# Optimization experiments

Measured on AMD Instinct MI355X. Metric: run time of the kernel, lower is better.

## Reference

```python
import jax, jax.numpy as jnp
import numpy as np
from jax import lax

EPS = 1e-5  # flax BatchNorm default epsilon


def _conv(x, w, b, padding='SAME'):
    y = lax.conv_general_dilated(x, w, (1, 1), padding,
                                 dimension_numbers=('NHWC', 'HWIO', 'NHWC'))
    return y + b


def _maxpool(x, window, strides):
    return lax.reduce_window(x, -jnp.inf, lax.max,
                             (1,) + window + (1,), (1,) + strides + (1,), 'SAME')


def _bn_train(x, scale, bias):
    # training-mode BatchNorm: batch statistics over N,H,W
    m = x.mean(axis=(0, 1, 2))
    v = x.var(axis=(0, 1, 2))
    return (x - m) * lax.rsqrt(v + EPS) * scale + bias


def _lstm(x, wx, wh, b, carry, reverse):
    # x: (B, T, D); flax LSTMCell gate order i, f, g, o; bias lives on the
    # hidden dense in flax but is an equivalent single additive term here.
    xs = jnp.swapaxes(x @ wx + b, 0, 1)  # (T, B, 4H), input GEMM hoisted out of scan

    def step(ch, xt):
        c, h = ch
        g = xt + h @ wh
        i, f, gg, o = jnp.split(g, 4, axis=-1)
        c = jax.nn.sigmoid(f) * c + jax.nn.sigmoid(i) * jnp.tanh(gg)
        h = jax.nn.sigmoid(o) * jnp.tanh(c)
        return (c, h), h

    carry, ys = lax.scan(step, carry, xs, reverse=reverse)
    return carry, jnp.swapaxes(ys, 0, 1)  # (B, T, H)


def _forward(x, conv1_w, conv1_b, conv2_w, conv2_b, conv3_w, conv3_b, bn1_s, bn1_b,
             conv4_w, conv4_b, bn2_s, bn2_b, conv5_w, conv5_b, bn3_s, bn3_b,
             conv6_w, conv6_b, bn4_s, bn4_b, conv7_w, conv7_b, bn5_s, bn5_b,
             wq, bq, wk, bk, wv, bv,
             l1f_wx, l1f_wh, l1f_b, l1r_wx, l1r_wh, l1r_b,
             l2f_wx, l2f_wh, l2f_b, l2r_wx, l2r_wh, l2r_b, wo, bo):
    x = jax.nn.relu(_conv(x, conv1_w, conv1_b))
    x = _maxpool(x, (2, 2), (2, 2))
    x = jax.nn.relu(_conv(x, conv2_w, conv2_b))
    x = _maxpool(x, (2, 2), (2, 2))
    x = jax.nn.relu(_bn_train(_conv(x, conv3_w, conv3_b), bn1_s, bn1_b))
    x = jax.nn.relu(_bn_train(_conv(x, conv4_w, conv4_b), bn2_s, bn2_b))
    x = _maxpool(x, (2, 2), (1, 2))
    x = jax.nn.relu(_bn_train(_conv(x, conv5_w, conv5_b), bn3_s, bn3_b))
    x = jax.nn.relu(_bn_train(_conv(x, conv6_w, conv6_b), bn4_s, bn4_b))
    x = _maxpool(x, (2, 2), (1, 2))
    x = jax.nn.relu(_bn_train(_conv(x, conv7_w, conv7_b, padding='VALID'), bn5_s, bn5_b))
    B = x.shape[0]
    x = x.reshape(B, x.shape[1], -1)  # (B, T=H', W'*512); seq axis is height
    q = x @ wq + bq
    k = x @ wk + bk
    v = x @ wv + bv
    qk = jax.nn.softmax(jnp.einsum('btk,bsk->bts', q, k) / 32.0, axis=-1)
    x = jnp.einsum('btk,bts->bsk', v, qk)
    # stack 1: reverse LSTM deliberately starts from forward's FINAL carry (as in source)
    carry = (jnp.zeros((B, 256), x.dtype), jnp.zeros((B, 256), x.dtype))
    carry, y1 = _lstm(x, l1f_wx, l1f_wh, l1f_b, carry, reverse=False)
    carry, y2 = _lstm(x, l1r_wx, l1r_wh, l1r_b, carry, reverse=True)
    x1 = jnp.concatenate([y1, y2], axis=-1)
    # stack 2
    carry = (jnp.zeros((B, 512), x.dtype), jnp.zeros((B, 512), x.dtype))
    carry, y2b = _lstm(x1, l2f_wx, l2f_wh, l2f_b, carry, reverse=False)
    carry, y3 = _lstm(x1, l2r_wx, l2r_wh, l2r_b, carry, reverse=True)
    x = jnp.concatenate([y3, y2b], axis=-1)
    return x @ wo + bo


def setup_inputs() -> dict:
    key = jax.random.key(0)
    ks = iter(jax.random.split(key, 64))

    def cw(kh, kw, ci, co):
        return jax.random.normal(next(ks), (kh, kw, ci, co), jnp.float32) / np.float32(np.sqrt(kh * kw * ci))

    def dw(i, o):
        return jax.random.normal(next(ks), (i, o), jnp.float32) / np.float32(np.sqrt(i))

    z = lambda *s: jnp.zeros(s, jnp.float32)
    ones = lambda *s: jnp.ones(s, jnp.float32)
    class_nums = 1000
    d_in = 15 * 512  # W'=15 after conv stack, 512 channels
    inp = {
        'x': jax.random.normal(next(ks), (32, 64, 256, 3), jnp.float32),
        'conv1_w': cw(3, 3, 3, 64), 'conv1_b': z(64),
        'conv2_w': cw(3, 3, 64, 128), 'conv2_b': z(128),
        'conv3_w': cw(3, 3, 128, 256), 'conv3_b': z(256), 'bn1_s': ones(256), 'bn1_b': z(256),
        'conv4_w': cw(3, 3, 256, 256), 'conv4_b': z(256), 'bn2_s': ones(256), 'bn2_b': z(256),
        'conv5_w': cw(3, 3, 256, 512), 'conv5_b': z(512), 'bn3_s': ones(512), 'bn3_b': z(512),
        'conv6_w': cw(3, 3, 512, 512), 'conv6_b': z(512), 'bn4_s': ones(512), 'bn4_b': z(512),
        'conv7_w': cw(2, 2, 512, 512), 'conv7_b': z(512), 'bn5_s': ones(512), 'bn5_b': z(512),
        'wq': dw(d_in, 512), 'bq': z(512),
        'wk': dw(d_in, 512), 'bk': z(512),
        'wv': dw(d_in, 512), 'bv': z(512),
        'l1f_wx': dw(512, 4 * 256), 'l1f_wh': dw(256, 4 * 256), 'l1f_b': z(4 * 256),
        'l1r_wx': dw(512, 4 * 256), 'l1r_wh': dw(256, 4 * 256), 'l1r_b': z(4 * 256),
        'l2f_wx': dw(512, 4 * 512), 'l2f_wh': dw(512, 4 * 512), 'l2f_b': z(4 * 512),
        'l2r_wx': dw(512, 4 * 512), 'l2r_wh': dw(512, 4 * 512), 'l2r_b': z(4 * 512),
        'wo': dw(1024, class_nums), 'bo': z(class_nums),
    }
    return inp


def reference(x, conv1_w, conv1_b, conv2_w, conv2_b, conv3_w, conv3_b, bn1_s, bn1_b,
              conv4_w, conv4_b, bn2_s, bn2_b, conv5_w, conv5_b, bn3_s, bn3_b,
              conv6_w, conv6_b, bn4_s, bn4_b, conv7_w, conv7_b, bn5_s, bn5_b,
              wq, bq, wk, bk, wv, bv,
              l1f_wx, l1f_wh, l1f_b, l1r_wx, l1r_wh, l1r_b,
              l2f_wx, l2f_wh, l2f_b, l2r_wx, l2r_wh, l2r_b, wo, bo):
    return _forward(x, conv1_w, conv1_b, conv2_w, conv2_b, conv3_w, conv3_b, bn1_s, bn1_b,
                    conv4_w, conv4_b, bn2_s, bn2_b, conv5_w, conv5_b, bn3_s, bn3_b,
                    conv6_w, conv6_b, bn4_s, bn4_b, conv7_w, conv7_b, bn5_s, bn5_b,
                    wq, bq, wk, bk, wv, bv,
                    l1f_wx, l1f_wh, l1f_b, l1r_wx, l1r_wh, l1r_b,
                    l2f_wx, l2f_wh, l2f_b, l2r_wx, l2r_wh, l2r_b, wo, bo)
```

## Files before the change

### kernel.cpp

```cpp
#include <hip/hip_runtime.h>
#include <math.h>

#define DIV_UP(a,b) (((a)+(b)-1)/(b))

typedef _Float16 half_t;
typedef _Float16 half8 __attribute__((ext_vector_type(8)));
typedef float f32x4 __attribute__((ext_vector_type(4)));

#define FLAG_RELU   1
#define FLAG_OUTF32 2
#define FLAG_SPLITK 4
#define FLAG_ATOMIC 8
#define FLAG_BNSUMS 16

#define GLDS16(src, dst) \
  __builtin_amdgcn_global_load_lds((const __attribute__((address_space(1))) void*)(src), \
                                   (__attribute__((address_space(3))) void*)(dst), 16, 0, 0)

__device__ __forceinline__ float fsig_(float x){ return 1.0f/(1.0f+__expf(-x)); }
__device__ __forceinline__ float ftanh_(float x){
  float ax = fabsf(x);
  float e = __expf(-2.0f*ax);
  float t = (1.0f - e)/(1.0f + e);
  return copysignf(t, x);
}

#define NTP 18
struct TpAll {
  const float* src[NTP];
  half_t* dst[NTP];
  int K[NTP];
  int N[NTP];
  int prefix[NTP+1];
};

__global__ __launch_bounds__(256) void transpose_cvt_all_kernel(TpAll a)
{
  __shared__ float tile[32][33];
  int bid = blockIdx.x;
  int z = 0;
  while (bid >= a.prefix[z+1]) ++z;
  int local = bid - a.prefix[z];
  const float* w = a.src[z];
  half_t* wT = a.dst[z];
  int K = a.K[z], N = a.N[z];
  int tilesX = (N + 31) >> 5;
  int nt = (local % tilesX) * 32;
  int kt = (local / tilesX) * 32;
  int tx = threadIdx.x & 31, ty = threadIdx.x >> 5;
  #pragma unroll
  for (int r = 0; r < 4; ++r) {
    int k = kt + ty + r*8, n = nt + tx;
    tile[ty + r*8][tx] = (k < K && n < N) ? w[(long)k*N + n] : 0.f;
  }
  __syncthreads();
  #pragma unroll
  for (int r = 0; r < 4; ++r) {
    int n = nt + ty + r*8, k = kt + tx;
    if (n < N && k < K) wT[(long)n*K + k] = (half_t)tile[tx][ty + r*8];
  }
}

__global__ __launch_bounds__(256) void conv1_kernel(
    const float* __restrict__ x, const float* __restrict__ w,
    const float* __restrict__ bias, half_t* __restrict__ out)
{
  __shared__ float xs[3][258*3];
  int nb = blockIdx.x;
  int n = nb >> 6, ho = nb & 63;
  int tid = threadIdx.x;
  int co = tid & 63;
  float wreg[27];
  #pragma unroll
  for (int k = 0; k < 27; ++k) wreg[k] = w[k*64 + co];
  float bco = bias[co];
  for (int i = tid; i < 3*258*3; i += 256) {
    int row = i / (258*3); int rem = i % (258*3);
    int col = rem / 3;     int ci  = rem % 3;
    int ih = ho - 1 + row; int iw = col - 1;
    float v = 0.f;
    if (ih >= 0 && ih < 64 && iw >= 0 && iw < 256)
      v = x[(((long)n*64 + ih)*256 + iw)*3 + ci];
    xs[row][col*3 + ci] = v;
  }
  __syncthreads();
  int wave = tid >> 6;
  for (int p = 0; p < 64; ++p) {
    int wo = wave*64 + p;
    float acc = bco;
    #pragma unroll
    for (int kh = 0; kh < 3; ++kh)
      #pragma unroll
      for (int kw = 0; kw < 3; ++kw)
        #pragma unroll
        for (int ci = 0; ci < 3; ++ci)
          acc = fmaf(xs[kh][(wo+kw)*3 + ci], wreg[(kh*3+kw)*3 + ci], acc);
    acc = fmaxf(acc, 0.f);
    out[(((long)n*64 + ho)*256 + wo)*64 + co] = (half_t)acc;
  }
}

struct GOut { const half_t* wT; const float* bias; void* out; };

__global__ __launch_bounds__(256) void mfma_conv_kernel(
    const half_t* __restrict__ x, GOut g0, GOut g1, GOut g2,
    const half_t* __restrict__ zbuf, float* __restrict__ bns,
    int N,int H,int W,int Ci,int Ho,int Wo,int Co,
    int KH,int KW,int padH,int padW,
    int M,int K,int flags,int splitS)
{
  GOut g;
  int ciBeg = 0, ciEnd = Ci;
  if (flags & FLAG_SPLITK) {
    g = g0;
    int span = Ci / splitS;
    ciBeg = blockIdx.z * span;
    ciEnd = ciBeg + span;
  } else {
    g = (blockIdx.z == 0) ? g0 : (blockIdx.z == 1 ? g1 : g2);
  }
  const half_t* __restrict__ wT = g.wT;
  __shared__ half_t As[128*64];
  __shared__ half_t Bs[128*64];
  int tid = threadIdx.x;

  int nbx = gridDim.x, nby = gridDim.y;
  int total = nbx * nby;
  int flat = blockIdx.y * nbx + blockIdx.x;
  int q = total >> 3, r = total & 7;
  int xcd = flat & 7;
  int j = flat >> 3;
  int w = xcd * q + (xcd < r ? xcd : r) + j;
  int m0 = (w / nbx) * 128, n0 = (w % nbx) * 128;

  int wave = tid >> 6, lane = tid & 63;
  int l15 = lane & 15, quad = lane >> 4;
  int x7 = lane & 7;
  int wm = (wave & 1) * 64, wn = (wave >> 1) * 64;

  int rSub = tid >> 3;
  int colHalf = (((tid & 7) ^ (rSub & 7))) * 8;

  int ho_[4], wo_[4], ni_[4]; bool av_[4];
  #pragma unroll
  for (int i = 0; i < 4; ++i) {
    int m = m0 + i*32 + rSub;
    av_[i] = m < M;
    int mm = av_[i] ? m : 0;
    wo_[i] = mm % Wo; int t2 = mm / Wo;
    ho_[i] = t2 % Ho; ni_[i] = t2 / Ho;
  }
  const half_t* bBase[4];
  #pragma unroll
  for (int i = 0; i < 4; ++i) {
    int n = n0 + i*32 + rSub;
    bBase[i] = (n < Co) ? (wT + (long)n*K + colHalf) : nullptr;
  }

  int pch0 = ((quad)     ^ x7) * 8;
  int pch1 = ((4 + quad) ^ x7) * 8;

  f32x4 acc[4][4];
  #pragma unroll
  for (int i = 0; i < 4; ++i)
    #pragma unroll
    for (int j2 = 0; j2 < 4; ++j2)
      acc[i][j2] = (f32x4){0.f, 0.f, 0.f, 0.f};

  int kg = ciBeg;
  for (int kh = 0; kh < KH; ++kh) {
    for (int kw = 0; kw < KW; ++kw) {
      long aOff[4]; bool aval[4];
      #pragma unroll
      for (int i = 0; i < 4; ++i) {
        int ih = ho_[i] - padH + kh, iw = wo_[i] - padW + kw;
        bool ok = av_[i] && ih >= 0 && ih < H && iw >= 0 && iw < W;
        aval[i] = ok;
        aOff[i] = ok ? ((((long)ni_[i]*H + ih)*W + iw)*(long)Ci + colHalf) : 0;
      }
      for (int ci = ciBeg; ci < ciEnd; ci += 64, kg += 64) {
        #pragma unroll
        for (int i = 0; i < 4; ++i) {
          const half_t* sa = aval[i] ? (x + aOff[i] + ci) : zbuf;
          GLDS16(sa, As + i*2048 + wave*512);
          const half_t* sb = bBase[i] ? (bBase[i] + kg) : zbuf;
          GLDS16(sb, Bs + i*2048 + wave*512);
        }
        __syncthreads();
        {
          half8 af[4], bf[4];
          #pragma unroll
          for (int i = 0; i < 4; ++i)
            af[i] = *reinterpret_cast<half8*>(&As[(wm + i*16 + l15)*64 + pch0]);
          #pragma unroll
          for (int j2 = 0; j2 < 4; ++j2)
            bf[j2] = *reinterpret_cast<half8*>(&Bs[(wn + j2*16 + l15)*64 + pch0]);
          #pragma unroll
          for (int i = 0; i < 4; ++i)
            #pragma unroll
            for (int j2 = 0; j2 < 4; ++j2)
              acc[i][j2] = __builtin_amdgcn_mfma_f32_16x16x32_f16(af[i], bf[j2], acc[i][j2], 0, 0, 0);
        }
        {
          half8 af[4], bf[4];
          #pragma unroll
          for (int i = 0; i < 4; ++i)
            af[i] = *reinterpret_cast<half8*>(&As[(wm + i*16 + l15)*64 + pch1]);
          #pragma unroll
          for (int j2 = 0; j2 < 4; ++j2)
            bf[j2] = *reinterpret_cast<half8*>(&Bs[(wn + j2*16 + l15)*64 + pch1]);
          #pragma unroll
          for (int i = 0; i < 4; ++i)
            #pragma unroll
            for (int j2 = 0; j2 < 4; ++j2)
              acc[i][j2] = __builtin_amdgcn_mfma_f32_16x16x32_f16(af[i], bf[j2], acc[i][j2], 0, 0, 0);
        }
        __syncthreads();
      }
    }
  }

  if (flags & FLAG_BNSUMS) {
    float* red = (float*)As;
    #pragma unroll
    for (int j2 = 0; j2 < 4; ++j2) {
      int n = n0 + wn + j2*16 + l15;
      float bv = g.bias[n];
      float s = 0.f, qq = 0.f;
      #pragma unroll
      for (int i = 0; i < 4; ++i)
        #pragma unroll
        for (int rr = 0; rr < 4; ++rr) {
          int m = m0 + wm + i*16 + quad*4 + rr;
          if (m < M) { float v = acc[i][j2][rr] + bv; s += v; qq += v*v; }
        }
      int idx = ((((wave*4 + quad)*16 + l15)*4) + j2)*2;
      red[idx] = s; red[idx+1] = qq;
    }
    __syncthreads();
    if (tid < 128) {
      int hi = tid >> 6;
      int jj = (tid >> 4) & 3, ll = tid & 15;
      float s = 0.f, qq = 0.f;
      #pragma unroll
      for (int w2 = 0; w2 < 2; ++w2)
        #pragma unroll
        for (int qd = 0; qd < 4; ++qd) {
          int idx = (((((hi*2 + w2)*4 + qd)*16 + ll)*4) + jj)*2;
          s += red[idx]; qq += red[idx+1];
        }
      int n = n0 + tid;
      atomicAdd(&bns[n], s);
      atomicAdd(&bns[Co + n], qq);
    }
  }

  #pragma unroll
  for (int i = 0; i < 4; ++i) {
    #pragma unroll
    for (int rr = 0; rr < 4; ++rr) {
      int m = m0 + wm + i*16 + quad*4 + rr;
      if (m >= M) continue;
      #pragma unroll
      for (int j2 = 0; j2 < 4; ++j2) {
        int n = n0 + wn + j2*16 + l15;
        if (n >= Co) continue;
        if (flags & FLAG_ATOMIC) {
          atomicAdd(&((float*)g.out)[(long)m*Co + n], acc[i][j2][rr]);
        } else {
          float v = acc[i][j2][rr] + g.bias[n];
          if (flags & FLAG_RELU) v = fmaxf(v, 0.f);
          if (flags & FLAG_OUTF32) ((float*)g.out)[(long)m*Co + n] = v;
          else ((half_t*)g.out)[(long)m*Co + n] = (half_t)v;
        }
      }
    }
  }
}

__global__ __launch_bounds__(256) void maxpool8_kernel(
    const half_t* __restrict__ x, half_t* __restrict__ out,
    int N,int H,int W,int C,int Ho,int Wo,int sH,int sW)
{
  int C8 = C >> 3;
  long idx = (long)blockIdx.x*256 + threadIdx.x;
  long total8 = (long)N*Ho*Wo*C8;
  if (idx >= total8) return;
  int cb = (int)(idx % C8);
  long pix = idx / C8;
  int wo = (int)(pix % Wo); long t2 = pix / Wo;
  int ho = (int)(t2 % Ho); int n = (int)(t2 / Ho);
  int c = cb * 8;
  float m[8];
  #pragma unroll
  for (int e = 0; e < 8; ++e) m[e] = -INFINITY;
  for (int i = 0; i < 2; ++i) {
    int ih = ho*sH + i;
    if (ih >= H) continue;
    for (int j = 0; j < 2; ++j) {
      int iw = wo*sW + j;
      if (iw >= W) continue;
      half8 v = *reinterpret_cast<const half8*>(x + (((long)n*H + ih)*W + iw)*C + c);
      #pragma unroll
      for (int e = 0; e < 8; ++e) m[e] = fmaxf(m[e], (float)v[e]);
    }
  }
  half8 o;
  #pragma unroll
  for (int e = 0; e < 8; ++e) o[e] = (half_t)m[e];
  *reinterpret_cast<half8*>(out + idx*8) = o;
}

__global__ __launch_bounds__(256) void bn_apply_relu8_kernel(
    half_t* __restrict__ x, const float* __restrict__ sums,
    const float* __restrict__ scale, const float* __restrict__ bias,
    long total8, int C, float invN)
{
  long idx = (long)blockIdx.x*256 + threadIdx.x;
  if (idx >= total8) return;
  int c = (int)((idx*8) % C);
  half8 v = *reinterpret_cast<half8*>(x + idx*8);
  half8 o;
  #pragma unroll
  for (int e = 0; e < 8; ++e) {
    float mean = sums[c+e] * invN;
    float var  = sums[C + c+e] * invN - mean*mean;
    float rstd = rsqrtf(var + 1e-5f);
    float y = ((float)v[e] - mean) * rstd * scale[c+e] + bias[c+e];
    o[e] = (half_t)fmaxf(y, 0.0f);
  }
  *reinterpret_cast<half8*>(x + idx*8) = o;
}

__global__ __launch_bounds__(256) void bn_pool8_kernel(
    const half_t* __restrict__ x, half_t* __restrict__ out,
    const float* __restrict__ sums, const float* __restrict__ scale,
    const float* __restrict__ bias,
    int N,int H,int W,int C,int Ho,int Wo,int sH,int sW, float invN)
{
  int C8 = C >> 3;
  long idx = (long)blockIdx.x*256 + threadIdx.x;
  long total8 = (long)N*Ho*Wo*C8;
  if (idx >= total8) return;
  int cb = (int)(idx % C8);
  long pix = idx / C8;
  int wo = (int)(pix % Wo); long t2 = pix / Wo;
  int ho = (int)(t2 % Ho); int n = (int)(t2 / Ho);
  int c = cb * 8;
  float mean[8], rs[8], bb[8];
  #pragma unroll
  for (int e = 0; e < 8; ++e) {
    mean[e] = sums[c+e] * invN;
    float var = sums[C + c+e] * invN - mean[e]*mean[e];
    rs[e] = rsqrtf(var + 1e-5f) * scale[c+e];
    bb[e] = bias[c+e];
  }
  float m[8];
  #pragma unroll
  for (int e = 0; e < 8; ++e) m[e] = -INFINITY;
  for (int i = 0; i < 2; ++i) {
    int ih = ho*sH + i;
    if (ih >= H) continue;
    for (int j = 0; j < 2; ++j) {
      int iw = wo*sW + j;
      if (iw >= W) continue;
      half8 v = *reinterpret_cast<const half8*>(x + (((long)n*H + ih)*W + iw)*C + c);
      #pragma unroll
      for (int e = 0; e < 8; ++e) {
        float y = fmaxf(((float)v[e] - mean[e]) * rs[e] + bb[e], 0.f);
        m[e] = fmaxf(m[e], y);
      }
    }
  }
  half8 o;
  #pragma unroll
  for (int e = 0; e < 8; ++e) o[e] = (half_t)m[e];
  *reinterpret_cast<half8*>(out + idx*8) = o;
}

__global__ __launch_bounds__(256) void bias_fill_kernel(
    float* __restrict__ out, const float* __restrict__ b0,
    const float* __restrict__ b1, const float* __restrict__ b2, int total)
{
  int idx = blockIdx.x*256 + threadIdx.x;
  if (idx >= total) return;
  int n = idx % 1536;
  float v = (n < 512) ? b0[n] : (n < 1024 ? b1[n-512] : b2[n-1024]);
  out[idx] = v;
}

__global__ __launch_bounds__(256) void attention_kernel(
    const float* __restrict__ qkv, half_t* __restrict__ out,
    int T, int D, int ld)
{
  int b = blockIdx.x;
  int tid = threadIdx.x;
  __shared__ float P[15][16];
  if (tid < T*T) {
    int t = tid / T, s = tid % T;
    const float* qp = qkv + ((long)b*T + t)*ld;
    const float* kp = qkv + ((long)b*T + s)*ld + 512;
    float acc = 0.f;
    for (int d = 0; d < D; d += 4) {
      float4 qv = *reinterpret_cast<const float4*>(qp + d);
      float4 kv = *reinterpret_cast<const float4*>(kp + d);
      acc += qv.x*kv.x + qv.y*kv.y + qv.z*kv.z + qv.w*kv.w;
    }
    P[t][s] = acc * (1.0f/32.0f);
  }
  __syncthreads();
  if (tid < T) {
    float mx = -INFINITY;
    for (int s = 0; s < T; ++s) mx = fmaxf(mx, P[tid][s]);
    float sum = 0.f;
    for (int s = 0; s < T; ++s) { float e = expf(P[tid][s] - mx); P[tid][s] = e; sum += e; }
    float inv = 1.0f / sum;
    for (int s = 0; s < T; ++s) P[tid][s] *= inv;
  }
  __syncthreads();
  for (int idx = tid; idx < T*D; idx += 256) {
    int s = idx / D, kk2 = idx % D;
    float acc = 0.f;
    #pragma unroll
    for (int t = 0; t < 15; ++t)
      acc += qkv[((long)b*T + t)*ld + 1024 + kk2] * P[t][s];
    out[((long)b*T + s)*D + kk2] = (half_t)acc;
  }
}

#define MAXK 512
#define HSROW (MAXK + 8)

template<int N64, int HLOG>
__device__ __forceinline__ void stage_h(
    const unsigned long long* __restrict__ src, half_t (*hs)[HSROW], int tid)
{
  unsigned long long tmp[N64];
  #pragma unroll
  for (int u = 0; u < N64; ++u)
    tmp[u] = __hip_atomic_load(src + tid + u*256, __ATOMIC_RELAXED, __HIP_MEMORY_SCOPE_AGENT);
  #pragma unroll
  for (int u = 0; u < N64; ++u) {
    int idx = tid + u*256;
    int row = idx >> (HLOG - 2);
    int col = (idx & ((1 << (HLOG - 2)) - 1)) * 4;
    *reinterpret_cast<unsigned long long*>(&hs[row][col]) = tmp[u];
  }
}

template<int H>
__global__ __launch_bounds__(256, 1) void lstm_persistent_kernel(
    const float* __restrict__ preF, const float* __restrict__ preR,
    const half_t* __restrict__ whTF, const half_t* __restrict__ whTR,
    half_t* __restrict__ hbuf, half_t* __restrict__ y,
    int* __restrict__ flags, int nblk,
    int ystride, int yoffF, int yoffR)
{
  constexpr int KI = H / 32;
  __shared__ half_t hs[32][HSROW];
  __shared__ float gates[32][133];
  int tid = threadIdx.x;
  int jb0 = blockIdx.x * 32;
  int lane = tid & 63, wave = tid >> 6;
  int l15 = lane & 15, quad = lane >> 4;
  int bb = tid >> 3;
  int jj0 = (tid & 7) * 4;
  constexpr int H4 = 4 * H;

  float cst[4] = {0.f, 0.f, 0.f, 0.f};
  half8 wreg[2][KI];

  auto loadw = [&](const half_t* __restrict__ whT) {
    #pragma unroll
    for (int f = 0; f < 2; ++f) {
      const half_t* wp = whT + (long)(wave*H + jb0 + f*16 + l15)*H + quad*8;
      #pragma unroll
      for (int i = 0; i < KI; ++i)
        wreg[f][i] = *reinterpret_cast<const half8*>(wp + i*32);
    }
  };

  auto loadpv = [&](int s, float (&pv)[16]) {
    const float* pr = (s < 15) ? preF : preR;
    int t = (s < 15) ? s : 29 - s;
    const float* pp = pr + (long)(bb*15 + t)*H4 + jb0 + jj0;
    #pragma unroll
    for (int g = 0; g < 4; ++g) {
      f32x4 v = *reinterpret_cast<const f32x4*>(pp + g*H);
      pv[g*4+0] = v[0]; pv[g*4+1] = v[1]; pv[g*4+2] = v[2]; pv[g*4+3] = v[3];
    }
  };

  loadw(whTF);
  float pv[16];
  loadpv(0, pv);

  for (int s = 0; s < 30; ++s) {
    if (s == 15) loadw(whTR);
    int t = (s < 15) ? s : 29 - s;
    int yoff = (s < 15) ? yoffF : yoffR;

    const unsigned long long* hsrc =
        (const unsigned long long*)(hbuf + (long)(s & 1) * 32 * H);
    if constexpr (H == 512) stage_h<16, 9>(hsrc, hs, tid);
    else                    stage_h<8, 8>(hsrc, hs, tid);
    __syncthreads();

    f32x4 acc00 = {0.f,0.f,0.f,0.f}, acc10 = {0.f,0.f,0.f,0.f};
    f32x4 acc01 = {0.f,0.f,0.f,0.f}, acc11 = {0.f,0.f,0.f,0.f};
    #pragma unroll
    for (int i = 0; i < KI; ++i) {
      half8 a0 = *reinterpret_cast<half8*>(&hs[l15][i*32 + quad*8]);
      half8 a1 = *reinterpret_cast<half8*>(&hs[16 + l15][i*32 + quad*8]);
      acc00 = __builtin_amdgcn_mfma_f32_16x16x32_f16(a0, wreg[0][i], acc00, 0, 0, 0);
      acc10 = __builtin_amdgcn_mfma_f32_16x16x32_f16(a1, wreg[0][i], acc10, 0, 0, 0);
      acc01 = __builtin_amdgcn_mfma_f32_16x16x32_f16(a0, wreg[1][i], acc01, 0, 0, 0);
      acc11 = __builtin_amdgcn_mfma_f32_16x16x32_f16(a1, wreg[1][i], acc11, 0, 0, 0);
    }
    #pragma unroll
    for (int r = 0; r < 4; ++r) {
      gates[quad*4 + r][wave*32 + l15]           = acc00[r];
      gates[16 + quad*4 + r][wave*32 + l15]      = acc10[r];
      gates[quad*4 + r][wave*32 + 16 + l15]      = acc01[r];
      gates[16 + quad*4 + r][wave*32 + 16 + l15] = acc11[r];
    }
    __syncthreads();

    unsigned long long hpack;
    {
      half_t hn[4];
      #pragma unroll
      for (int p = 0; p < 4; ++p) {
        int j = jj0 + p;
        float gi = pv[p]      + gates[bb][j];
        float gf = pv[4 + p]  + gates[bb][32 + j];
        float gg = pv[8 + p]  + gates[bb][64 + j];
        float go = pv[12 + p] + gates[bb][96 + j];
        gi = fsig_(gi); gf = fsig_(gf); gg = ftanh_(gg); go = fsig_(go);
        float cn = gf * cst[p] + gi * gg;
        cst[p] = cn;
        hn[p] = (half_t)(go * ftanh_(cn));
      }
      hpack = *reinterpret_cast<unsigned long long*>(hn);
      half_t* hdst = hbuf + (long)((s + 1) & 1) * 32 * H;
      __hip_atomic_store((unsigned long long*)(hdst + (long)bb*H + jb0 + jj0), hpack,
                         __ATOMIC_RELAXED, __HIP_MEMORY_SCOPE_AGENT);
    }

    if (s < 29) {
      __syncthreads();
      if (tid == 0)
        __hip_atomic_store(&flags[blockIdx.x], s + 1,
                           __ATOMIC_RELAXED, __HIP_MEMORY_SCOPE_AGENT);
      *reinterpret_cast<unsigned long long*>(
          &y[(long)(bb*15 + t)*ystride + yoff + jb0 + jj0]) = hpack;
      loadpv(s + 1, pv);
      if (tid < 64) {
        int target = s + 1;
        for (;;) {
          int vv = (tid < nblk)
            ? __hip_atomic_load(&flags[tid], __ATOMIC_RELAXED, __HIP_MEMORY_SCOPE_AGENT)
            : target;
          if (__all(vv >= target)) break;
        }
      }
      __syncthreads();
    } else {
      *reinterpret_cast<unsigned long long*>(
          &y[(long)(bb*15 + t)*ystride + yoff + jb0 + jj0]) = hpack;
    }
  }
}

extern "C" void kernel_launch(void* const* d_in, const int* in_sizes, int n_in,
                              void* d_out, int out_size, void* d_ws, size_t ws_size,
                              hipStream_t stream)
{
  const float* x       = (const float*)d_in[0];
  const float* c1w     = (const float*)d_in[1];  const float* c1b = (const float*)d_in[2];
  const float* c2w     = (const float*)d_in[3];  const float* c2b = (const float*)d_in[4];
  const float* c3w     = (const float*)d_in[5];  const float* c3b = (const float*)d_in[6];
  const float* bn1s    = (const float*)d_in[7];  const float* bn1b = (const float*)d_in[8];
  const float* c4w     = (const float*)d_in[9];  const float* c4b = (const float*)d_in[10];
  const float* bn2s    = (const float*)d_in[11]; const float* bn2b = (const float*)d_in[12];
  const float* c5w     = (const float*)d_in[13]; const float* c5b = (const float*)d_in[14];
  const float* bn3s    = (const float*)d_in[15]; const float* bn3b = (const float*)d_in[16];
  const float* c6w     = (const float*)d_in[17]; const float* c6b = (const float*)d_in[18];
  const float* bn4s    = (const float*)d_in[19]; const float* bn4b = (const float*)d_in[20];
  const float* c7w     = (const float*)d_in[21]; const float* c7b = (const float*)d_in[22];
  const float* bn5s    = (const float*)d_in[23]; const float* bn5b = (const float*)d_in[24];
  const float* wq      = (const float*)d_in[25]; const float* bq = (const float*)d_in[26];
  const float* wk      = (const float*)d_in[27]; const float* bk = (const float*)d_in[28];
  const float* wv      = (const float*)d_in[29]; const float* bv = (const float*)d_in[30];
  const float* l1f_wx  = (const float*)d_in[31]; const float* l1f_wh = (const float*)d_in[32]; const float* l1f_b = (const float*)d_in[33];
  const float* l1r_wx  = (const float*)d_in[34]; const float* l1r_wh = (const float*)d_in[35]; const float* l1r_b = (const float*)d_in[36];
  const float* l2f_wx  = (const float*)d_in[37]; const float* l2f_wh = (const float*)d_in[38]; const float* l2f_b = (const float*)d_in[39];
  const float* l2r_wx  = (const float*)d_in[40]; const float* l2r_wh = (const float*)d_in[41]; const float* l2r_b = (const float*)d_in[42];
  const float* wo      = (const float*)d_in[43]; const float* bo = (const float*)d_in[44];
  float* outp = (float*)d_out;

  char* base = (char*)d_ws;
  half_t* actA = (half_t*)base;
  half_t* actB = (half_t*)(base + 67108864);
  half_t* wtA  = (half_t*)(base + 100663296);
  float*  f32a = (float*)(base + 143687680);
  half_t* h16a = (half_t*)(base + 158736384);

  half_t* wt2  = wtA;
  half_t* wt3  = wtA + 73728;
  half_t* wt4  = wtA + 368640;
  half_t* wt5  = wtA + 958464;
  half_t* wt6  = wtA + 2138112;
  half_t* wt7  = wtA + 4497408;
  half_t* wtq  = wtA + 5545984;
  half_t* wtk  = wtA + 9478144;
  half_t* wtv  = wtA + 13410304;
  half_t* wt1f = wtA + 17342464;
  half_t* wt1r = wtA + 17866752;
  half_t* wt2f = wtA + 18391040;
  half_t* wt2r = wtA + 19439616;
  half_t* wto  = wtA + 20488192;

  float* qkvbuf = f32a;
  float* pre1f = f32a + 737280;
  float* pre1r = f32a + 1228800;
  float* pre2f = f32a + 1720320;
  float* pre2r = f32a + 2703360;

  half_t* ao  = h16a;
  half_t* x1  = h16a + 245760;
  half_t* x2  = h16a + 491520;
  half_t* hb1 = h16a + 983040;
  half_t* hb2 = hb1 + 16384;
  int*    flags1 = (int*)(hb2 + 32768);
  int*    flags2 = flags1 + 512;
  half_t* zbuf   = (half_t*)(flags2 + 512);
  float*  bnz    = (float*)(zbuf + 32);

  half_t* whT1f = (half_t*)(base + 160849920);
  half_t* whT1r = (half_t*)(base + 161374208);
  half_t* whT2f = (half_t*)(base + 161898496);
  half_t* whT2r = (half_t*)(base + 163995648);

  auto convm = [&](const half_t* in, const half_t* wt, const float* b, void* out,
                   int N,int H,int W,int Ci,int Ho,int Wo,int Co,
                   int KH,int KW,int pH,int pW,int flags, float* bns){
    int M = N*Ho*Wo, K = KH*KW*Ci;
    dim3 grid(DIV_UP(Co,128), DIV_UP(M,128), 1);
    GOut g{wt, b, out};
    mfma_conv_kernel<<<grid,256,0,stream>>>(in,g,g,g,zbuf,bns,N,H,W,Ci,Ho,Wo,Co,
                                            KH,KW,pH,pW,M,K,flags,1);
  };
  auto gemm3 = [&](const half_t* A, GOut g0, GOut g1, GOut g2, int nz,
                   int M, int Nn, int K, int flags, int splitS){
    dim3 grid(DIV_UP(Nn,128), DIV_UP(M,128), nz);
    mfma_conv_kernel<<<grid,256,0,stream>>>(A,g0,g1,g2,zbuf,bnz,M,1,1,K,1,1,Nn,
                                            1,1,0,0,M,K,flags,splitS);
  };
  auto pool = [&](const half_t* in, half_t* out, int N,int H,int W,int C,
                  int Ho,int Wo,int sH,int sW){
    long total8 = (long)N*Ho*Wo*(C/8);
    maxpool8_kernel<<<(int)DIV_UP(total8,256),256,0,stream>>>(in,out,N,H,W,C,Ho,Wo,sH,sW);
  };
  auto bnApply = [&](half_t* buf, long nPix, int C, const float* s, const float* b,
                     float* sums){
    long total8 = nPix * C / 8;
    bn_apply_relu8_kernel<<<(int)DIV_UP(total8,256),256,0,stream>>>(buf, sums, s, b, total8, C, 1.0f/(float)nPix);
  };
  auto bnPool = [&](const half_t* in, half_t* out, int N,int H,int W,int C,
                    int Ho,int Wo,int sH,int sW, long nPix,
                    const float* s, const float* b, float* sums){
    long total8 = (long)N*Ho*Wo*(C/8);
    bn_pool8_kernel<<<(int)DIV_UP(total8,256),256,0,stream>>>(
        in,out,sums,s,b,N,H,W,C,Ho,Wo,sH,sW,1.0f/(float)nPix);
  };

  hipMemsetAsync(hb1, 0, 143424, stream);

  {
    TpAll tp;
    const float* srcs[NTP] = {c2w,c3w,c4w,c5w,c6w,c7w,wq,wk,wv,l1f_wx,l1r_wx,l2f_wx,l2r_wx,wo,
                              l1f_wh,l1r_wh,l2f_wh,l2r_wh};
    half_t* dsts[NTP] = {wt2,wt3,wt4,wt5,wt6,wt7,wtq,wtk,wtv,wt1f,wt1r,wt2f,wt2r,wto,
                         whT1f,whT1r,whT2f,whT2r};
    int Ks[NTP] = {576,1152,2304,2304,4608,2048,7680,7680,7680,512,512,512,512,1024,
                   256,256,512,512};
    int Ns[NTP] = {128,256,256,512,512,512,512,512,512,1024,1024,2048,2048,1000,
                   1024,1024,2048,2048};
    int acc = 0;
    for (int i = 0; i < NTP; ++i) {
      tp.src[i] = srcs[i]; tp.dst[i] = dsts[i]; tp.K[i] = Ks[i]; tp.N[i] = Ns[i];
      tp.prefix[i] = acc;
      acc += DIV_UP(Ks[i],32) * DIV_UP(Ns[i],32);
    }
    tp.prefix[NTP] = acc;
    transpose_cvt_all_kernel<<<acc,256,0,stream>>>(tp);
  }

  conv1_kernel<<<2048,256,0,stream>>>(x, c1w, c1b, actA);
  pool(actA, actB, 32,64,256,64,  32,128, 2,2);
  convm(actB, wt2, c2b, actA, 32,32,128,64,  32,128,128, 3,3,1,1, FLAG_RELU, bnz);
  pool(actA, actB, 32,32,128,128, 16,64, 2,2);
  convm(actB, wt3, c3b, actA, 32,16,64,128,  16,64,256,  3,3,1,1, FLAG_BNSUMS, bnz);
  bnApply(actA, 32768, 256, bn1s, bn1b, bnz);
  convm(actA, wt4, c4b, actB, 32,16,64,256,  16,64,256,  3,3,1,1, FLAG_BNSUMS, bnz + 2048);
  bnPool(actB, actA, 32,16,64,256, 16,32, 1,2, 32768, bn2s, bn2b, bnz + 2048);
  convm(actA, wt5, c5b, actB, 32,16,32,256,  16,32,512,  3,3,1,1, FLAG_BNSUMS, bnz + 4096);
  bnApply(actB, 16384, 512, bn3s, bn3b, bnz + 4096);
  convm(actB, wt6, c6b, actA, 32,16,32,512,  16,32,512,  3,3,1,1, FLAG_BNSUMS, bnz + 6144);
  bnPool(actA, actB, 32,16,32,512, 16,16, 1,2, 16384, bn4s, bn4b, bnz + 6144);
  convm(actB, wt7, c7b, actA, 32,16,16,512,  15,15,512,  2,2,0,0, FLAG_BNSUMS, bnz + 8192);
  bnApply(actA, 7200, 512, bn5s, bn5b, bnz + 8192);

  bias_fill_kernel<<<DIV_UP(480*1536,256),256,0,stream>>>(qkvbuf, bq, bk, bv, 480*1536);
  gemm3(actA, GOut{wtq, nullptr, qkvbuf}, GOut{wtq, nullptr, qkvbuf},
        GOut{wtq, nullptr, qkvbuf}, 4, 480, 1536, 7680, FLAG_SPLITK|FLAG_ATOMIC, 4);
  attention_kernel<<<32,256,0,stream>>>(qkvbuf, ao, 15, 512, 1536);

  gemm3(ao, GOut{wt1f, l1f_b, pre1f}, GOut{wt1r, l1r_b, pre1r},
        GOut{wt1r, l1r_b, pre1r}, 2, 480, 1024, 512, FLAG_OUTF32, 1);
  lstm_persistent_kernel<256><<<8,256,0,stream>>>(
      pre1f, pre1r, whT1f, whT1r, hb1, x1, flags1, 8, 512, 0, 256);

  gemm3(x1, GOut{wt2f, l2f_b, pre2f}, GOut{wt2r, l2r_b, pre2r},
        GOut{wt2r, l2r_b, pre2r}, 2, 480, 2048, 512, FLAG_OUTF32, 1);
  lstm_persistent_kernel<512><<<16,256,0,stream>>>(
      pre2f, pre2r, whT2f, whT2r, hb2, x2, flags2, 16, 1024, 512, 0);

  gemm3(x2, GOut{wto, bo, outp}, GOut{wto, bo, outp}, GOut{wto, bo, outp}, 1,
        480, 1000, 1024, FLAG_OUTF32, 1);
}
```

Before: 1.050 ms.

## Double-buffer LDS tiles in MFMA conv kernel to overlap loads with compute

Converts the implicit-GEMM conv main loop to a flattened K-tile loop with two LDS buffers for A and B. The next tile's global-to-LDS loads are issued before the MFMA work on the current tile, and one barrier per iteration replaces two. This aims to hide global memory latency behind the matrix math. In exchange LDS use doubles to 64KB per block, which may lower occupancy. The single barrier relies on the async LDS loads being complete before the buffer is read, which is a correctness risk.

```diff
diff --git a/kernel.cpp b/kernel.cpp
--- a/kernel.cpp
+++ b/kernel.cpp
@@ -120,8 +120,8 @@
     g = (blockIdx.z == 0) ? g0 : (blockIdx.z == 1 ? g1 : g2);
   }
   const half_t* __restrict__ wT = g.wT;
-  __shared__ half_t As[128*64];
-  __shared__ half_t Bs[128*64];
+  __shared__ half_t As[2][128*64];
+  __shared__ half_t Bs[2][128*64];
   int tid = threadIdx.x;
 
   int nbx = gridDim.x, nby = gridDim.y;
@@ -167,57 +167,73 @@
     for (int j2 = 0; j2 < 4; ++j2)
       acc[i][j2] = (f32x4){0.f, 0.f, 0.f, 0.f};
 
-  int kg = ciBeg;
-  for (int kh = 0; kh < KH; ++kh) {
-    for (int kw = 0; kw < KW; ++kw) {
-      long aOff[4]; bool aval[4];
-      #pragma unroll
-      for (int i = 0; i < 4; ++i) {
-        int ih = ho_[i] - padH + kh, iw = wo_[i] - padW + kw;
-        bool ok = av_[i] && ih >= 0 && ih < H && iw >= 0 && iw < W;
-        aval[i] = ok;
-        aOff[i] = ok ? ((((long)ni_[i]*H + ih)*W + iw)*(long)Ci + colHalf) : 0;
-      }
-      for (int ci = ciBeg; ci < ciEnd; ci += 64, kg += 64) {
+  int NT = ((ciEnd - ciBeg) >> 6) * KH * KW;
+  int skh = 0, skw = 0, sci = ciBeg;
+  long sAOff[4]; bool sAval[4];
+  auto recompA = [&]() {
+    #pragma unroll
+    for (int i = 0; i < 4; ++i) {
+      int ih = ho_[i] - padH + skh, iw = wo_[i] - padW + skw;
+      bool ok = av_[i] && ih >= 0 && ih < H && iw >= 0 && iw < W;
+      sAval[i] = ok;
+      sAOff[i] = ok ? ((((long)ni_[i]*H + ih)*W + iw)*(long)Ci + colHalf) : 0;
+    }
+  };
+  recompA();
+  auto stage = [&](int b) {
+    int kgS = (skh*KW + skw)*Ci + sci;
+    #pragma unroll
+    for (int i = 0; i < 4; ++i) {
+      const half_t* sa = sAval[i] ? (x + sAOff[i] + sci) : zbuf;
+      GLDS16(sa, &As[b][i*2048 + wave*512]);
+      const half_t* sb = bBase[i] ? (bBase[i] + kgS) : zbuf;
+      GLDS16(sb, &Bs[b][i*2048 + wave*512]);
+    }
+  };
+  auto advance = [&]() {
+    sci += 64;
+    if (sci == ciEnd) {
+      sci = ciBeg; ++skw;
+      if (skw == KW) { skw = 0; ++skh; }
+      recompA();
+    }
+  };
+
+  stage(0); advance();
+  __syncthreads();
+
+  for (int kt = 0; kt < NT; ++kt) {
+    int p = kt & 1;
+    if (kt + 1 < NT) { stage(p ^ 1); advance(); }
+    {
+      half8 af[4], bf[4];
+      #pragma unroll
+      for (int i = 0; i < 4; ++i)
+        af[i] = *reinterpret_cast<half8*>(&As[p][(wm + i*16 + l15)*64 + pch0]);
+      #pragma unroll
+      for (int j2 = 0; j2 < 4; ++j2)
+        bf[j2] = *reinterpret_cast<half8*>(&Bs[p][(wn + j2*16 + l15)*64 + pch0]);
+      #pragma unroll
+      for (int i = 0; i < 4; ++i)
         #pragma unroll
-        for (int i = 0; i < 4; ++i) {
-          const half_t* sa = aval[i] ? (x + aOff[i] + ci) : zbuf;
-          GLDS16(sa, As + i*2048 + wave*512);
-          const half_t* sb = bBase[i] ? (bBase[i] + kg) : zbuf;
-          GLDS16(sb, Bs + i*2048 + wave*512);
-        }
-        __syncthreads();
-        {
-          half8 af[4], bf[4];
-          #pragma unroll
-          for (int i = 0; i < 4; ++i)
-            af[i] = *reinterpret_cast<half8*>(&As[(wm + i*16 + l15)*64 + pch0]);
-          #pragma unroll
-          for (int j2 = 0; j2 < 4; ++j2)
-            bf[j2] = *reinterpret_cast<half8*>(&Bs[(wn + j2*16 + l15)*64 + pch0]);
-          #pragma unroll
-          for (int i = 0; i < 4; ++i)
-            #pragma unroll
-            for (int j2 = 0; j2 < 4; ++j2)
-              acc[i][j2] = __builtin_amdgcn_mfma_f32_16x16x32_f16(af[i], bf[j2], acc[i][j2], 0, 0, 0);
-        }
-        {
-          half8 af[4], bf[4];
-          #pragma unroll
-          for (int i = 0; i < 4; ++i)
-            af[i] = *reinterpret_cast<half8*>(&As[(wm + i*16 + l15)*64 + pch1]);
-          #pragma unroll
-          for (int j2 = 0; j2 < 4; ++j2)
-            bf[j2] = *reinterpret_cast<half8*>(&Bs[(wn + j2*16 + l15)*64 + pch1]);
-          #pragma unroll
-          for (int i = 0; i < 4; ++i)
-            #pragma unroll
-            for (int j2 = 0; j2 < 4; ++j2)
-              acc[i][j2] = __builtin_amdgcn_mfma_f32_16x16x32_f16(af[i], bf[j2], acc[i][j2], 0, 0, 0);
-        }
-        __syncthreads();
-      }
-    }
+        for (int j2 = 0; j2 < 4; ++j2)
+          acc[i][j2] = __builtin_amdgcn_mfma_f32_16x16x32_f16(af[i], bf[j2], acc[i][j2], 0, 0, 0);
+    }
+    {
+      half8 af[4], bf[4];
+      #pragma unroll
+      for (int i = 0; i < 4; ++i)
+        af[i] = *reinterpret_cast<half8*>(&As[p][(wm + i*16 + l15)*64 + pch1]);
+      #pragma unroll
+      for (int j2 = 0; j2 < 4; ++j2)
+        bf[j2] = *reinterpret_cast<half8*>(&Bs[p][(wn + j2*16 + l15)*64 + pch1]);
+      #pragma unroll
+      for (int i = 0; i < 4; ++i)
+        #pragma unroll
+        for (int j2 = 0; j2 < 4; ++j2)
+          acc[i][j2] = __builtin_amdgcn_mfma_f32_16x16x32_f16(af[i], bf[j2], acc[i][j2], 0, 0, 0);
+    }
+    __syncthreads();
   }
 
   if (flags & FLAG_BNSUMS) {
```

Result: no change. 1.041 ms (-0.8%).
